# Kernel optimization log

Hardware: AMD Instinct MI355X
Metric: run time of the kernel (lower is better)

Reference implementation:

```python
import jax, jax.numpy as jnp
import numpy as np

B, S, NQ, FFN, EMB = 8, 4096, 8, 2048, 512


def setup_inputs() -> dict:
    key = jax.random.key(0)
    k0, k1, k2, k3 = jax.random.split(key, 4)
    x = jax.random.normal(k0, (B, S, NQ), dtype=jnp.float32)
    theta = jax.random.normal(k1, (NQ,), dtype=jnp.float32)  # trainable RY angles
    W1 = jax.random.normal(k2, (NQ, FFN), dtype=jnp.float32) / np.float32(np.sqrt(NQ))
    b1 = jnp.zeros((FFN,), dtype=jnp.float32)
    W2 = jax.random.normal(k3, (FFN, EMB), dtype=jnp.float32) / np.float32(np.sqrt(FFN))
    b2 = jnp.zeros((EMB,), dtype=jnp.float32)
    return {"x": x, "theta": theta, "W1": W1, "b1": b1, "W2": W2, "b2": b2}


def reference(x, theta, W1, b1, W2, b2):
    # Quantum layer: per wire i, state RY(theta_i) RX(x_i) |0>; no entangling gates,
    # so the state is a product state and <PauliZ_i> = cos(x_i) * cos(theta_i) exactly.
    # This fuses the per-token / per-gate simulation loop into one batched expression.
    q = jnp.cos(x) * jnp.cos(theta)                     # [B, S, NQ]
    # Dropout is identity at eval time.
    h = jax.nn.relu(jnp.einsum("bsq,qf->bsf", q, W1) + b1)  # [B, S, FFN]
    out = jnp.einsum("bsf,fe->bse", h, W2) + b2             # [B, S, EMB]
    return out
```

## Files before the change

### kernel.cpp

```cpp
#include <hip/hip_runtime.h>

#define T_TOK 32768
#define NQ    8
#define FFN   2048
#define EMB   512
#define BM    128
#define BN    128
#define BK    32
#define NCHUNK (FFN / BK)

typedef __attribute__((ext_vector_type(8)))  short short8;
typedef __attribute__((ext_vector_type(16))) float f32x16;
typedef __attribute__((ext_vector_type(2)))  unsigned int u32x2;

__device__ __forceinline__ unsigned short f2bf(float f) {
  unsigned int u = __float_as_uint(f);
  u += 0x7fffu + ((u >> 16) & 1u);
  return (unsigned short)(u >> 16);
}

__device__ __forceinline__ unsigned pk2bf(float lo, float hi) {
#if __has_builtin(__builtin_amdgcn_cvt_pk_bf16_f32)
  typedef __attribute__((ext_vector_type(2))) __bf16 bf2;
  bf2 p = __builtin_amdgcn_cvt_pk_bf16_f32(lo, hi);
  return *(unsigned*)&p;
#else
  return (unsigned)f2bf(lo) | ((unsigned)f2bf(hi) << 16);
#endif
}

__global__ void prep_all(const float* __restrict__ W1,
                         const float* __restrict__ b1,
                         const float* __restrict__ W2,
                         unsigned short* __restrict__ w1t,
                         unsigned short* __restrict__ w2f) {
  __shared__ float t[32][33];
  const int kb  = blockIdx.x * 32;
  const int nb  = blockIdx.y * 32;
  const int tid = threadIdx.x;
  const int c = tid & 31, r0 = tid >> 5;
#pragma unroll
  for (int p = 0; p < 4; ++p)
    t[r0 + p * 8][c] = W2[(size_t)(kb + r0 + p * 8) * EMB + nb + c];
  __syncthreads();
  {
    const int ks = tid >> 7;
    const int hh = (tid >> 6) & 1;
    const int cc = (tid >> 1) & 31;
    const int e0 = (tid & 1) * 4;
    ushort4 v;
    v.x = f2bf(t[ks * 16 + hh * 8 + e0 + 0][cc]);
    v.y = f2bf(t[ks * 16 + hh * 8 + e0 + 1][cc]);
    v.z = f2bf(t[ks * 16 + hh * 8 + e0 + 2][cc]);
    v.w = f2bf(t[ks * 16 + hh * 8 + e0 + 3][cc]);
    *(ushort4*)(w2f + (size_t)(blockIdx.y * NCHUNK + blockIdx.x) * 1024 +
                tid * 4) = v;
  }
  if (blockIdx.x == 0) {
    const int f     = blockIdx.y * 128 + (tid >> 1);
    const int khalf = tid & 1;
    unsigned short v8[8];
#pragma unroll
    for (int j = 0; j < 8; ++j) {
      const int k = khalf * 8 + j;
      float val = (k < 8) ? W1[(size_t)k * FFN + f]
                          : (k == 8 ? b1[f] : 0.f);
      v8[j] = f2bf(val);
    }
    *(uint4*)(w1t + (size_t)f * 16 + khalf * 8) = *(uint4*)v8;
  }
}

__global__ __launch_bounds__(256, 4) void ffq_main(
    const float* __restrict__ x,
    const float* __restrict__ theta,
    const unsigned short* __restrict__ w1t,
    const unsigned short* __restrict__ w2f,
    const float* __restrict__ b2,
    float* __restrict__ out) {

  const int tid  = threadIdx.x;
  const int wave = tid >> 6;
  const int lane = tid & 63;
  const int nl   = lane & 31;
  const int hi   = lane >> 5;
  const int tok0 = blockIdx.x * BM;
  const int nt0  = blockIdx.y * 4;

  float cth[8];
  {
    const float4* tp = (const float4*)theta;
    float4 t0 = tp[0], t1 = tp[1];
    cth[0] = __cosf(t0.x); cth[1] = __cosf(t0.y);
    cth[2] = __cosf(t0.z); cth[3] = __cosf(t0.w);
    cth[4] = __cosf(t1.x); cth[5] = __cosf(t1.y);
    cth[6] = __cosf(t1.z); cth[7] = __cosf(t1.w);
  }
  short8 bq;
  {
    const float4* xp =
        (const float4*)(x + (size_t)(tok0 + wave * 32 + nl) * NQ);
    float4 x0 = xp[0], x1 = xp[1];
    float q0 = __cosf(x0.x) * cth[0], q1 = __cosf(x0.y) * cth[1];
    float q2 = __cosf(x0.z) * cth[2], q3 = __cosf(x0.w) * cth[3];
    float q4 = __cosf(x1.x) * cth[4], q5 = __cosf(x1.y) * cth[5];
    float q6 = __cosf(x1.z) * cth[6], q7 = __cosf(x1.w) * cth[7];
    uint4 uu;
    uu.x = pk2bf(q0, q1); uu.y = pk2bf(q2, q3);
    uu.z = pk2bf(q4, q5); uu.w = pk2bf(q6, q7);
    if (hi) { uu.x = 0x00003f80u; uu.y = 0; uu.z = 0; uu.w = 0; }
    bq = *(short8*)&uu;
  }

  const unsigned short* w2fl = w2f + (size_t)lane * 8;

  f32x16 acc[4];
#pragma unroll
  for (int nt = 0; nt < 4; ++nt)
#pragma unroll
    for (int r = 0; r < 16; ++r) acc[nt][r] = 0.f;

  auto gemm1 = [&](int kcx, short8& oA, short8& oB) {
    short8 aw = *(const short8*)(w1t + (size_t)(kcx * BK + nl) * 16 + hi * 8);
    f32x16 c1;
#pragma unroll
    for (int r = 0; r < 16; ++r) c1[r] = 0.f;
    c1 = __builtin_amdgcn_mfma_f32_32x32x16_bf16(aw, bq, c1, 0, 0, 0);
    unsigned Q[8];
#pragma unroll
    for (int p = 0; p < 8; ++p) {
      float lo = c1[2 * p]     > 0.f ? c1[2 * p]     : 0.f;
      float hl = c1[2 * p + 1] > 0.f ? c1[2 * p + 1] : 0.f;
      Q[p] = pk2bf(lo, hl);
    }
    u32x2 s0 = __builtin_amdgcn_permlane32_swap(Q[0], Q[2], false, false);
    u32x2 s1 = __builtin_amdgcn_permlane32_swap(Q[1], Q[3], false, false);
    u32x2 s2 = __builtin_amdgcn_permlane32_swap(Q[4], Q[6], false, false);
    u32x2 s3 = __builtin_amdgcn_permlane32_swap(Q[5], Q[7], false, false);
    uint4 uA; uA.x = s0[0]; uA.y = s1[0]; uA.z = s0[1]; uA.w = s1[1];
    uint4 uB; uB.x = s2[0]; uB.y = s3[0]; uB.z = s2[1]; uB.w = s3[1];
    oA = *(short8*)&uA;
    oB = *(short8*)&uB;
  };

  short8 afA_c, afB_c, afA_n, afB_n;
  gemm1(0, afA_c, afB_c);

#pragma unroll 2
  for (int kc = 0; kc < NCHUNK; ++kc) {
    const int nc   = (kc + 1 < NCHUNK) ? kc + 1 : NCHUNK - 1;
    const int base = (nt0 * NCHUNK + kc) * 1024;

    short8 bf0 = *(const short8*)(w2fl + base);
    short8 bf1 = *(const short8*)(w2fl + base + 1 * NCHUNK * 1024);
    short8 bf2 = *(const short8*)(w2fl + base + 2 * NCHUNK * 1024);
    short8 bf3 = *(const short8*)(w2fl + base + 3 * NCHUNK * 1024);

    gemm1(nc, afA_n, afB_n);

    acc[0] = __builtin_amdgcn_mfma_f32_32x32x16_bf16(afA_c, bf0, acc[0], 0, 0, 0);
    acc[1] = __builtin_amdgcn_mfma_f32_32x32x16_bf16(afA_c, bf1, acc[1], 0, 0, 0);
    acc[2] = __builtin_amdgcn_mfma_f32_32x32x16_bf16(afA_c, bf2, acc[2], 0, 0, 0);
    acc[3] = __builtin_amdgcn_mfma_f32_32x32x16_bf16(afA_c, bf3, acc[3], 0, 0, 0);

    bf0 = *(const short8*)(w2fl + base + 512);
    bf1 = *(const short8*)(w2fl + base + 1 * NCHUNK * 1024 + 512);
    bf2 = *(const short8*)(w2fl + base + 2 * NCHUNK * 1024 + 512);
    bf3 = *(const short8*)(w2fl + base + 3 * NCHUNK * 1024 + 512);

    acc[0] = __builtin_amdgcn_mfma_f32_32x32x16_bf16(afB_c, bf0, acc[0], 0, 0, 0);
    acc[1] = __builtin_amdgcn_mfma_f32_32x32x16_bf16(afB_c, bf1, acc[1], 0, 0, 0);
    acc[2] = __builtin_amdgcn_mfma_f32_32x32x16_bf16(afB_c, bf2, acc[2], 0, 0, 0);
    acc[3] = __builtin_amdgcn_mfma_f32_32x32x16_bf16(afB_c, bf3, acc[3], 0, 0, 0);

    afA_c = afA_n;
    afB_c = afB_n;
  }

#pragma unroll
  for (int nt = 0; nt < 4; ++nt) {
    const int col = (nt0 + nt) * 32 + nl;
    const float bv = b2[col];
    const int rbase = tok0 + wave * 32 + 4 * hi;
#pragma unroll
    for (int g2 = 0; g2 < 4; ++g2)
#pragma unroll
      for (int rr = 0; rr < 4; ++rr)
        out[(size_t)(rbase + 8 * g2 + rr) * EMB + col] =
            acc[nt][4 * g2 + rr] + bv;
  }
}

extern "C" void kernel_launch(void* const* d_in, const int* in_sizes, int n_in,
                              void* d_out, int out_size, void* d_ws, size_t ws_size,
                              hipStream_t stream) {
  const float* x     = (const float*)d_in[0];
  const float* theta = (const float*)d_in[1];
  const float* W1    = (const float*)d_in[2];
  const float* b1    = (const float*)d_in[3];
  const float* W2    = (const float*)d_in[4];
  const float* b2    = (const float*)d_in[5];
  float* out = (float*)d_out;

  unsigned short* w1t = (unsigned short*)d_ws;
  unsigned short* w2f = w1t + FFN * 16;

  prep_all<<<dim3(FFN / 32, EMB / 32), 256, 0, stream>>>(W1, b1, W2, w1t, w2f);

  dim3 grid(T_TOK / BM, EMB / BN);
  ffq_main<<<grid, 256, 0, stream>>>(x, theta, w1t, w2f, b2, out);
}
```

Baseline: 188.7 us.

## Widen output tile to 256 columns per block to amortize GEMM1 recompute

Each block now covers 256 output columns (8 MFMA accumulator tiles per wave) instead of 128, halving the grid's y-dimension. The first GEMM (q·W1 plus ReLU) is recomputed per block, so wider tiles halve that redundant work and the cos/x loads. The cost is doubled accumulator registers (128 floats per lane) and fewer waves per SIMD, with launch bounds lowered to 2 blocks. All 16 W2 fragment loads are now issued up front each iteration.

```diff
diff --git a/kernel.cpp b/kernel.cpp
--- a/kernel.cpp
+++ b/kernel.cpp
@@ -5,7 +5,7 @@
 #define FFN   2048
 #define EMB   512
 #define BM    128
-#define BN    128
+#define BN    256
 #define BK    32
 #define NCHUNK (FFN / BK)
 
@@ -71,7 +71,7 @@
   }
 }
 
-__global__ __launch_bounds__(256, 4) void ffq_main(
+__global__ __launch_bounds__(256, 2) void ffq_main(
     const float* __restrict__ x,
     const float* __restrict__ theta,
     const unsigned short* __restrict__ w1t,
@@ -85,7 +85,7 @@
   const int nl   = lane & 31;
   const int hi   = lane >> 5;
   const int tok0 = blockIdx.x * BM;
-  const int nt0  = blockIdx.y * 4;
+  const int nt0  = blockIdx.y * 8;
 
   float cth[8];
   {
@@ -113,15 +113,22 @@
   }
 
   const unsigned short* w2fl = w2f + (size_t)lane * 8;
-
-  f32x16 acc[4];
-#pragma unroll
-  for (int nt = 0; nt < 4; ++nt)
+  const unsigned short* p0 = w2fl + (size_t)(nt0 + 0) * NCHUNK * 1024;
+  const unsigned short* p1 = w2fl + (size_t)(nt0 + 1) * NCHUNK * 1024;
+  const unsigned short* p2 = w2fl + (size_t)(nt0 + 2) * NCHUNK * 1024;
+  const unsigned short* p3 = w2fl + (size_t)(nt0 + 3) * NCHUNK * 1024;
+  const unsigned short* p4 = w2fl + (size_t)(nt0 + 4) * NCHUNK * 1024;
+  const unsigned short* p5 = w2fl + (size_t)(nt0 + 5) * NCHUNK * 1024;
+  const unsigned short* p6 = w2fl + (size_t)(nt0 + 6) * NCHUNK * 1024;
+  const unsigned short* p7 = w2fl + (size_t)(nt0 + 7) * NCHUNK * 1024;
+
+  f32x16 acc[8];
+#pragma unroll
+  for (int nt = 0; nt < 8; ++nt)
 #pragma unroll
     for (int r = 0; r < 16; ++r) acc[nt][r] = 0.f;
 
-  auto gemm1 = [&](int kcx, short8& oA, short8& oB) {
-    short8 aw = *(const short8*)(w1t + (size_t)(kcx * BK + nl) * 16 + hi * 8);
+  auto gemm1 = [&](short8 aw, short8& oA, short8& oB) {
     f32x16 c1;
 #pragma unroll
     for (int r = 0; r < 16; ++r) c1[r] = 0.f;
@@ -144,41 +151,64 @@
   };
 
   short8 afA_c, afB_c, afA_n, afB_n;
-  gemm1(0, afA_c, afB_c);
+  {
+    short8 aw0 = *(const short8*)(w1t + (size_t)nl * 16 + hi * 8);
+    gemm1(aw0, afA_c, afB_c);
+  }
 
 #pragma unroll 2
   for (int kc = 0; kc < NCHUNK; ++kc) {
-    const int nc   = (kc + 1 < NCHUNK) ? kc + 1 : NCHUNK - 1;
-    const int base = (nt0 * NCHUNK + kc) * 1024;
-
-    short8 bf0 = *(const short8*)(w2fl + base);
-    short8 bf1 = *(const short8*)(w2fl + base + 1 * NCHUNK * 1024);
-    short8 bf2 = *(const short8*)(w2fl + base + 2 * NCHUNK * 1024);
-    short8 bf3 = *(const short8*)(w2fl + base + 3 * NCHUNK * 1024);
-
-    gemm1(nc, afA_n, afB_n);
-
-    acc[0] = __builtin_amdgcn_mfma_f32_32x32x16_bf16(afA_c, bf0, acc[0], 0, 0, 0);
-    acc[1] = __builtin_amdgcn_mfma_f32_32x32x16_bf16(afA_c, bf1, acc[1], 0, 0, 0);
-    acc[2] = __builtin_amdgcn_mfma_f32_32x32x16_bf16(afA_c, bf2, acc[2], 0, 0, 0);
-    acc[3] = __builtin_amdgcn_mfma_f32_32x32x16_bf16(afA_c, bf3, acc[3], 0, 0, 0);
-
-    bf0 = *(const short8*)(w2fl + base + 512);
-    bf1 = *(const short8*)(w2fl + base + 1 * NCHUNK * 1024 + 512);
-    bf2 = *(const short8*)(w2fl + base + 2 * NCHUNK * 1024 + 512);
-    bf3 = *(const short8*)(w2fl + base + 3 * NCHUNK * 1024 + 512);
-
-    acc[0] = __builtin_amdgcn_mfma_f32_32x32x16_bf16(afB_c, bf0, acc[0], 0, 0, 0);
-    acc[1] = __builtin_amdgcn_mfma_f32_32x32x16_bf16(afB_c, bf1, acc[1], 0, 0, 0);
-    acc[2] = __builtin_amdgcn_mfma_f32_32x32x16_bf16(afB_c, bf2, acc[2], 0, 0, 0);
-    acc[3] = __builtin_amdgcn_mfma_f32_32x32x16_bf16(afB_c, bf3, acc[3], 0, 0, 0);
+    const int nc = (kc + 1 < NCHUNK) ? kc + 1 : NCHUNK - 1;
+    const int kb = kc * 1024;
+
+    short8 b00 = *(const short8*)(p0 + kb);
+    short8 b10 = *(const short8*)(p1 + kb);
+    short8 b20 = *(const short8*)(p2 + kb);
+    short8 b30 = *(const short8*)(p3 + kb);
+    short8 b40 = *(const short8*)(p4 + kb);
+    short8 b50 = *(const short8*)(p5 + kb);
+    short8 b60 = *(const short8*)(p6 + kb);
+    short8 b70 = *(const short8*)(p7 + kb);
+
+    {
+      short8 aw =
+          *(const short8*)(w1t + (size_t)(nc * BK + nl) * 16 + hi * 8);
+      gemm1(aw, afA_n, afB_n);
+    }
+
+    short8 b01 = *(const short8*)(p0 + kb + 512);
+    short8 b11 = *(const short8*)(p1 + kb + 512);
+    short8 b21 = *(const short8*)(p2 + kb + 512);
+    short8 b31 = *(const short8*)(p3 + kb + 512);
+    short8 b41 = *(const short8*)(p4 + kb + 512);
+    short8 b51 = *(const short8*)(p5 + kb + 512);
+    short8 b61 = *(const short8*)(p6 + kb + 512);
+    short8 b71 = *(const short8*)(p7 + kb + 512);
+
+    acc[0] = __builtin_amdgcn_mfma_f32_32x32x16_bf16(afA_c, b00, acc[0], 0, 0, 0);
+    acc[1] = __builtin_amdgcn_mfma_f32_32x32x16_bf16(afA_c, b10, acc[1], 0, 0, 0);
+    acc[2] = __builtin_amdgcn_mfma_f32_32x32x16_bf16(afA_c, b20, acc[2], 0, 0, 0);
+    acc[3] = __builtin_amdgcn_mfma_f32_32x32x16_bf16(afA_c, b30, acc[3], 0, 0, 0);
+    acc[4] = __builtin_amdgcn_mfma_f32_32x32x16_bf16(afA_c, b40, acc[4], 0, 0, 0);
+    acc[5] = __builtin_amdgcn_mfma_f32_32x32x16_bf16(afA_c, b50, acc[5], 0, 0, 0);
+    acc[6] = __builtin_amdgcn_mfma_f32_32x32x16_bf16(afA_c, b60, acc[6], 0, 0, 0);
+    acc[7] = __builtin_amdgcn_mfma_f32_32x32x16_bf16(afA_c, b70, acc[7], 0, 0, 0);
+
+    acc[0] = __builtin_amdgcn_mfma_f32_32x32x16_bf16(afB_c, b01, acc[0], 0, 0, 0);
+    acc[1] = __builtin_amdgcn_mfma_f32_32x32x16_bf16(afB_c, b11, acc[1], 0, 0, 0);
+    acc[2] = __builtin_amdgcn_mfma_f32_32x32x16_bf16(afB_c, b21, acc[2], 0, 0, 0);
+    acc[3] = __builtin_amdgcn_mfma_f32_32x32x16_bf16(afB_c, b31, acc[3], 0, 0, 0);
+    acc[4] = __builtin_amdgcn_mfma_f32_32x32x16_bf16(afB_c, b41, acc[4], 0, 0, 0);
+    acc[5] = __builtin_amdgcn_mfma_f32_32x32x16_bf16(afB_c, b51, acc[5], 0, 0, 0);
+    acc[6] = __builtin_amdgcn_mfma_f32_32x32x16_bf16(afB_c, b61, acc[6], 0, 0, 0);
+    acc[7] = __builtin_amdgcn_mfma_f32_32x32x16_bf16(afB_c, b71, acc[7], 0, 0, 0);
 
     afA_c = afA_n;
     afB_c = afB_n;
   }
 
 #pragma unroll
-  for (int nt = 0; nt < 4; ++nt) {
+  for (int nt = 0; nt < 8; ++nt) {
     const int col = (nt0 + nt) * 32 + nl;
     const float bv = b2[col];
     const int rbase = tok0 + wave * 32 + 4 * hi;
```

New measurement: 183.0 us. 1.03x faster.
